# Optimization experiments

Hardware: AMD Instinct MI355X
Metric: run time of the kernel (lower is better)

Reference implementation:

```python
import jax, jax.numpy as jnp
import numpy as np
from jax import lax

EPS_OT = 0.05
N_ITERS = 100
NEG = -1e9

def _l2norm(x):
    n = jnp.sqrt(jnp.sum(x * x, axis=-1, keepdims=True))
    return x / jnp.maximum(n, 1e-12)

def _sinkhorn(C, mu, nu, mask):
    # C: (B, M, Nq); mu: (B, M); nu: (B, Nq); mask: (B, M) bool
    mrow = mask[:, :, None]   # masks rows of K (B,M,Nq)
    mcol = mask[:, None, :]   # masks cols of K^T (B,Nq,M)
    log_mu = jnp.log(mu + 1e-8)
    log_nu = jnp.log(nu + 1e-8)

    def kernel(u, v):
        return (-C + u[:, :, None] + v[:, None, :]) / EPS_OT

    def step(carry, _):
        u, v = carry
        K = jnp.where(mrow, kernel(u, v), NEG)
        u = EPS_OT * (log_mu - jax.scipy.special.logsumexp(K, axis=2)) + u
        Kt = jnp.where(mcol, jnp.transpose(kernel(u, v), (0, 2, 1)), NEG)
        v = EPS_OT * (log_nu - jax.scipy.special.logsumexp(Kt, axis=2)) + v
        return (u, v), None

    u0 = jnp.zeros_like(mu)
    v0 = jnp.zeros_like(nu)
    (u, v), _ = lax.scan(jax.checkpoint(step), (u0, v0), None, length=N_ITERS)
    K = jnp.where(mrow, kernel(u, v), NEG)
    T = jnp.exp(K)
    return jnp.where(mrow, T, 0.0)

def setup_inputs() -> dict:
    key = jax.random.key(0)
    ks = jax.random.split(key, 12)
    Nq, B, M, C = 1024, 8, 1024, 640
    s = 1.0 / np.sqrt(C)
    return {
        "xq": jax.random.normal(ks[0], (Nq, B, C), jnp.float32),
        "xk": jax.random.normal(ks[1], (B, M, C), jnp.float32),
        "xv": jax.random.normal(ks[2], (B, M, C), jnp.float32),
        "mask": jax.random.randint(ks[3], (B, M), 0, 2).astype(bool),
        "Wq": jax.random.normal(ks[4], (C, C), jnp.float32) * s,
        "bq": jnp.zeros((C,), jnp.float32),
        "Wk": jax.random.normal(ks[5], (C, C), jnp.float32) * s,
        "bk": jnp.zeros((C,), jnp.float32),
        "Wv": jax.random.normal(ks[6], (C, C), jnp.float32) * s,
        "bv": jnp.zeros((C,), jnp.float32),
        "Wp": jax.random.normal(ks[7], (C, C), jnp.float32) * s,
        "bp": jnp.zeros((C,), jnp.float32),
    }

def reference(xq, xk, xv, mask, Wq, bq, Wk, bk, Wv, bv, Wp, bp):
    Nq, B, C = xq.shape
    M = xk.shape[1]
    q = _l2norm(xq @ Wq.T + bq)          # (Nq, B, C)
    k = _l2norm(xk @ Wk.T + bk)          # (B, M, C)
    v = xv @ Wv.T + bv                   # (B, M, C)
    # einsum 'bmc,nbc->bnm' then permute(0,2,1) == direct (B, M, Nq)
    sim = jnp.einsum('bmc,nbc->bmn', k, q)
    wdist = 1.0 - sim
    counts = jnp.sum(mask, axis=1, keepdims=True).astype(sim.dtype)  # (B,1)
    xx = mask.astype(sim.dtype) / jnp.maximum(counts, 1.0)
    xx = jnp.where(counts == 0, 1.0 / M, xx)                         # (B, M)
    yy = jnp.full((B, Nq), 1.0 / Nq, sim.dtype)
    T = _sinkhorn(wdist, xx, yy, mask)                               # (B, M, Nq)
    score_map = (M * Nq) * sim * T
    attn_save = jnp.where(mask, jnp.sum(score_map, axis=-1), 0.0)    # (B, M)
    x = jnp.einsum('bmn,bmc->nbc', T, v)                             # (Nq, B, C)
    out = x @ Wp.T + bp
    return out, attn_save
```

## Files before the change

### kernel.cpp

```cpp
#include <hip/hip_runtime.h>
#include <cstdint>
#include <cstddef>

#define B_DIM 8
#define NQ    1024
#define MK    1024
#define CD    640
#define INV_EPS 20.0f
#define EPS_OT  0.05f

typedef unsigned short u16;
typedef __attribute__((ext_vector_type(8))) short bf16x8;
typedef __attribute__((ext_vector_type(4))) float f32x4;

#define GLDS(gp, lp) __builtin_amdgcn_global_load_lds( \
    (const __attribute__((address_space(1))) void*)(gp), \
    (__attribute__((address_space(3))) void*)(lp), 16, 0, 0)

static __device__ __forceinline__ float wave_reduce_sum(float s) {
#pragma unroll
  for (int off = 32; off; off >>= 1) s += __shfl_xor(s, off, 64);
  return s;
}

static __device__ __forceinline__ u16 f2bf(float f) {
  uint32_t u = __float_as_uint(f);
  u += 0x7fff + ((u >> 16) & 1);
  return (u16)(u >> 16);
}

static __device__ __forceinline__ void g_store(float* p, float v) {
  __hip_atomic_store(p, v, __ATOMIC_RELAXED, __HIP_MEMORY_SCOPE_AGENT);
}
static __device__ __forceinline__ float g_load(const float* p) {
  return __hip_atomic_load((float*)p, __ATOMIC_RELAXED, __HIP_MEMORY_SCOPE_AGENT);
}
static __device__ __forceinline__ void g_storeu(unsigned* p, unsigned v) {
  __hip_atomic_store(p, v, __ATOMIC_RELAXED, __HIP_MEMORY_SCOPE_AGENT);
}
static __device__ __forceinline__ unsigned g_loadu(const unsigned* p) {
  return __hip_atomic_load((unsigned*)p, __ATOMIC_RELAXED, __HIP_MEMORY_SCOPE_AGENT);
}

__global__ void k_setup(const void* __restrict__ maskRaw, int* __restrict__ maskI,
                        float* __restrict__ muVal, float* __restrict__ w,
                        unsigned* __restrict__ ctrl)
{
  __shared__ int s_flag;
  __shared__ int s_cnt[B_DIM];
  const int tid = threadIdx.x;
  if (tid == 0) s_flag = 0;
  if (tid < B_DIM) s_cnt[tid] = 0;
  ctrl[tid] = 0u;
  __syncthreads();

  const unsigned char* mb = (const unsigned char*)maskRaw;
  int local = 0;
  for (int i = tid; i < B_DIM * MK; i += 1024)
    if ((i & 3) && mb[i]) local = 1;
  if (local) atomicOr(&s_flag, 1);
  __syncthreads();

  const int isByte = s_flag;
  const int* mi32 = (const int*)maskRaw;
  for (int i = tid; i < B_DIM * MK; i += 1024) {
    int v = isByte ? (int)mb[i] : mi32[i];
    v = v ? 1 : 0;
    maskI[i] = v;
    if (v) atomicAdd(&s_cnt[i >> 10], 1);
  }
  for (int i = tid; i < B_DIM * NQ; i += 1024) w[i] = 1.0f;
  __syncthreads();
  if (tid < B_DIM) {
    float c = (float)s_cnt[tid];
    muVal[tid] = (c > 0.f ? 1.0f / c : 1.0f / (float)MK) + 1e-8f;
  }
}

__global__ __launch_bounds__(256)
void k_cvt5(const float* __restrict__ x0, u16* __restrict__ d0,
            const float* __restrict__ x1, u16* __restrict__ d1,
            const float* __restrict__ x2, u16* __restrict__ d2,
            const float* __restrict__ x3, u16* __restrict__ d3,
            const float* __restrict__ x4, u16* __restrict__ d4)
{
  const int a = blockIdx.y;
  const float* s; u16* d; int n;
  if      (a == 0) { s = x0; d = d0; n = 8192 * CD; }
  else if (a == 1) { s = x1; d = d1; n = 8192 * CD; }
  else if (a == 2) { s = x2; d = d2; n = 8192 * CD; }
  else if (a == 3) { s = x3; d = d3; n = CD * CD; }
  else             { s = x4; d = d4; n = CD * CD; }
  const int i = (blockIdx.x * 256 + threadIdx.x) * 4;
  if (i >= n) return;
  const float4 v = *(const float4*)(s + i);
  *(ushort4*)(d + i) = make_ushort4(f2bf(v.x), f2bf(v.y), f2bf(v.z), f2bf(v.w));
}

__global__ __launch_bounds__(256)
void k_combineA(const float* __restrict__ Wp, const float* __restrict__ Wv,
                u16* __restrict__ Ah)
{
  __shared__ float Ps[32][68];
  __shared__ float Vs[32][68];
  const int tid = threadIdx.x;
  const int c0 = blockIdx.x << 6, k0 = blockIdx.y << 6;
  const int ty = tid >> 4, tx = tid & 15;
  float acc[4][4];
#pragma unroll
  for (int i = 0; i < 4; ++i)
#pragma unroll
    for (int j = 0; j < 4; ++j) acc[i][j] = 0.f;

  for (int j0 = 0; j0 < CD; j0 += 32) {
    {
      const int c = tid >> 2, j4 = (tid & 3) << 3;
      const float* p = Wp + (size_t)(c0 + c) * CD + j0 + j4;
      float4 u0 = *(const float4*)p, u1 = *(const float4*)(p + 4);
      Ps[j4 + 0][c] = u0.x; Ps[j4 + 1][c] = u0.y; Ps[j4 + 2][c] = u0.z; Ps[j4 + 3][c] = u0.w;
      Ps[j4 + 4][c] = u1.x; Ps[j4 + 5][c] = u1.y; Ps[j4 + 6][c] = u1.z; Ps[j4 + 7][c] = u1.w;
    }
    {
      const int j = tid >> 3, k4 = (tid & 7) << 3;
      const float* p = Wv + (size_t)(j0 + j) * CD + k0 + k4;
      float4 u0 = *(const float4*)p, u1 = *(const float4*)(p + 4);
      *(float4*)&Vs[j][k4] = u0; *(float4*)&Vs[j][k4 + 4] = u1;
    }
    __syncthreads();
#pragma unroll
    for (int j = 0; j < 32; ++j) {
      float a[4], b[4];
      *(float4*)a = *(const float4*)&Ps[j][ty << 2];
      *(float4*)b = *(const float4*)&Vs[j][tx << 2];
#pragma unroll
      for (int i = 0; i < 4; ++i)
#pragma unroll
        for (int jj = 0; jj < 4; ++jj)
          acc[i][jj] = fmaf(a[i], b[jj], acc[i][jj]);
    }
    __syncthreads();
  }
#pragma unroll
  for (int i = 0; i < 4; ++i) {
    *(ushort4*)(Ah + (size_t)(c0 + (ty << 2) + i) * CD + k0 + (tx << 2)) =
      make_ushort4(f2bf(acc[i][0]), f2bf(acc[i][1]), f2bf(acc[i][2]), f2bf(acc[i][3]));
  }
}

__global__ __launch_bounds__(256)
void k_bvp(const float* __restrict__ Wp, const float* __restrict__ bv,
           float* __restrict__ bvp)
{
  const int c = (blockIdx.x << 2) + (threadIdx.x >> 6);
  const int lane = threadIdx.x & 63;
  float s = 0.f;
  for (int j = lane; j < CD; j += 64) s = fmaf(Wp[(size_t)c * CD + j], bv[j], s);
  s = wave_reduce_sum(s);
  if (!lane) bvp[c] = s;
}

__global__ __launch_bounds__(256)
void mfma_proj(const u16* __restrict__ xqh, const u16* __restrict__ xkh,
               const u16* __restrict__ xvh,
               const u16* __restrict__ Wqh, const u16* __restrict__ Wkh,
               const u16* __restrict__ Ah,
               const float* __restrict__ bq, const float* __restrict__ bk,
               const float* __restrict__ bvp,
               float* __restrict__ qb, float* __restrict__ kb,
               float* __restrict__ vp)
{
  __shared__ u16 As[128 * 32];
  __shared__ u16 Bs[128 * 32];
  const int mode = blockIdx.z;
  const u16* X     = (mode == 0) ? xqh : ((mode == 1) ? xkh : xvh);
  const u16* W     = (mode == 0) ? Wqh : ((mode == 1) ? Wkh : Ah);
  const float* bias= (mode == 0) ? bq  : ((mode == 1) ? bk  : bvp);
  float* outp      = (mode == 0) ? qb  : ((mode == 1) ? kb  : vp);

  const int tid = threadIdx.x, wave = tid >> 6, lane = tid & 63;
  const int row0 = blockIdx.x << 7, col0 = blockIdx.y << 7;

  const int rS = (wave << 5) + (lane >> 2);
  const int pc = lane & 3;
  const int kc0 = pc ^ ((rS >> 1) & 3);
  const int kc1 = pc ^ (((rS + 16) >> 1) & 3);
  const u16* gA0 = X + (size_t)(row0 + rS) * CD + (kc0 << 3);
  const u16* gA1 = X + (size_t)(row0 + rS + 16) * CD + (kc1 << 3);
  const u16* gB0 = W + (size_t)(col0 + rS) * CD + (kc0 << 3);
  const u16* gB1 = W + (size_t)(col0 + rS + 16) * CD + (kc1 << 3);
  u16* lA = As + (wave << 10);
  u16* lB = Bs + (wave << 10);

  const int wm0 = (wave & 1) << 6, wn0 = (wave >> 1) << 6;
  int aOff[4], bOff[4];
#pragma unroll
  for (int t = 0; t < 4; ++t) {
    const int ra = wm0 + (t << 4) + (lane & 15);
    aOff[t] = ra * 32 + (((lane >> 4) ^ ((ra >> 1) & 3)) << 3);
    const int rb = wn0 + (t << 4) + (lane & 15);
    bOff[t] = rb * 32 + (((lane >> 4) ^ ((rb >> 1) & 3)) << 3);
  }
  f32x4 acc[4][4];
#pragma unroll
  for (int i = 0; i < 4; ++i)
#pragma unroll
    for (int j = 0; j < 4; ++j) acc[i][j] = {0.f, 0.f, 0.f, 0.f};

  for (int k0 = 0; k0 < CD; k0 += 32) {
    __syncthreads();
    GLDS(gA0, lA); GLDS(gA1, lA + 512);
    GLDS(gB0, lB); GLDS(gB1, lB + 512);
    gA0 += 32; gA1 += 32; gB0 += 32; gB1 += 32;
    __syncthreads();
    bf16x8 a[4], b[4];
#pragma unroll
    for (int t = 0; t < 4; ++t) {
      a[t] = *(const bf16x8*)(As + aOff[t]);
      b[t] = *(const bf16x8*)(Bs + bOff[t]);
    }
#pragma unroll
    for (int i = 0; i < 4; ++i)
#pragma unroll
      for (int j = 0; j < 4; ++j)
        acc[i][j] = __builtin_amdgcn_mfma_f32_16x16x32_bf16(a[i], b[j], acc[i][j], 0, 0, 0);
  }

  float bv4[4];
  int ccs[4];
#pragma unroll
  for (int j = 0; j < 4; ++j) {
    ccs[j] = col0 + wn0 + (j << 4) + (lane & 15);
    bv4[j] = bias[ccs[j]];
  }
#pragma unroll
  for (int i = 0; i < 4; ++i) {
    const int rbase = row0 + wm0 + (i << 4) + ((lane >> 4) << 2);
#pragma unroll
    for (int r = 0; r < 4; ++r) {
      const int rr = rbase + r;
      const size_t orow = (mode == 0) ? ((size_t)(rr & 7) * NQ + (rr >> 3)) : (size_t)rr;
      float* op = outp + orow * CD;
#pragma unroll
      for (int j = 0; j < 4; ++j)
        op[ccs[j]] = acc[i][j][r] + bv4[j];
    }
  }
}

__global__ __launch_bounds__(256)
void mfma_sim(const u16* __restrict__ kbh, const u16* __restrict__ qbh,
              float* __restrict__ E)
{
  __shared__ u16 As[128 * 32];
  __shared__ u16 Bs[128 * 32];
  const int tid = threadIdx.x, wave = tid >> 6, lane = tid & 63;
  const int b = blockIdx.z;
  const int row0 = blockIdx.x << 7, col0 = blockIdx.y << 7;
  const u16* A = kbh + (size_t)b * MK * CD;
  const u16* B = qbh + (size_t)b * NQ * CD;

  const int rS = (wave << 5) + (lane >> 2);
  const int pc = lane & 3;
  const int kc0 = pc ^ ((rS >> 1) & 3);
  const int kc1 = pc ^ (((rS + 16) >> 1) & 3);
  const u16* gA0 = A + (size_t)(row0 + rS) * CD + (kc0 << 3);
  const u16* gA1 = A + (size_t)(row0 + rS + 16) * CD + (kc1 << 3);
  const u16* gB0 = B + (size_t)(col0 + rS) * CD + (kc0 << 3);
  const u16* gB1 = B + (size_t)(col0 + rS + 16) * CD + (kc1 << 3);
  u16* lA = As + (wave << 10);
  u16* lB = Bs + (wave << 10);

  const int wm0 = (wave & 1) << 6, wn0 = (wave >> 1) << 6;
  int aOff[4], bOff[4];
#pragma unroll
  for (int t = 0; t < 4; ++t) {
    const int ra = wm0 + (t << 4) + (lane & 15);
    aOff[t] = ra * 32 + (((lane >> 4) ^ ((ra >> 1) & 3)) << 3);
    const int rb = wn0 + (t << 4) + (lane & 15);
    bOff[t] = rb * 32 + (((lane >> 4) ^ ((rb >> 1) & 3)) << 3);
  }
  f32x4 acc[4][4];
#pragma unroll
  for (int i = 0; i < 4; ++i)
#pragma unroll
    for (int j = 0; j < 4; ++j) acc[i][j] = {0.f, 0.f, 0.f, 0.f};

  for (int k0 = 0; k0 < CD; k0 += 32) {
    __syncthreads();
    GLDS(gA0, lA); GLDS(gA1, lA + 512);
    GLDS(gB0, lB); GLDS(gB1, lB + 512);
    gA0 += 32; gA1 += 32; gB0 += 32; gB1 += 32;
    __syncthreads();
    bf16x8 a[4], b[4];
#pragma unroll
    for (int t = 0; t < 4; ++t) {
      a[t] = *(const bf16x8*)(As + aOff[t]);
      b[t] = *(const bf16x8*)(Bs + bOff[t]);
    }
#pragma unroll
    for (int i = 0; i < 4; ++i)
#pragma unroll
      for (int j = 0; j < 4; ++j)
        acc[i][j] = __builtin_amdgcn_mfma_f32_16x16x32_bf16(a[i], b[j], acc[i][j], 0, 0, 0);
  }

#pragma unroll
  for (int i = 0; i < 4; ++i) {
    const int rbase = row0 + wm0 + (i << 4) + ((lane >> 4) << 2);
#pragma unroll
    for (int r = 0; r < 4; ++r) {
      const int rr = rbase + r;
      float* erow = E + (((size_t)(b << 10) + rr) << 10);
#pragma unroll
      for (int j = 0; j < 4; ++j) {
        const int cc = col0 + wn0 + (j << 4) + (lane & 15);
        erow[cc] = __expf((acc[i][j][r] - 1.f) * INV_EPS);
      }
    }
  }
}

__global__ __launch_bounds__(256)
void mfma_x(const u16* __restrict__ Et, const u16* __restrict__ Vpt,
            const float* __restrict__ w, const float* __restrict__ bp,
            float* __restrict__ out)
{
  __shared__ u16 As[128 * 32];
  __shared__ u16 Bs[128 * 32];
  const int tid = threadIdx.x, wave = tid >> 6, lane = tid & 63;
  const int b = blockIdx.z;
  const int row0 = blockIdx.x << 7;
  const int col0 = blockIdx.y << 7;
  const u16* A = Et + ((size_t)b << 20);
  const u16* B = Vpt + (size_t)b * CD * MK;

  const int rS = (wave << 5) + (lane >> 2);
  const int pc = lane & 3;
  const int kc0 = pc ^ ((rS >> 1) & 3);
  const int kc1 = pc ^ (((rS + 16) >> 1) & 3);
  const u16* gA0 = A + ((size_t)(row0 + rS) << 10) + (kc0 << 3);
  const u16* gA1 = A + ((size_t)(row0 + rS + 16) << 10) + (kc1 << 3);
  const u16* gB0 = B + ((size_t)(col0 + rS) << 10) + (kc0 << 3);
  const u16* gB1 = B + ((size_t)(col0 + rS + 16) << 10) + (kc1 << 3);
  u16* lA = As + (wave << 10);
  u16* lB = Bs + (wave << 10);

  const int wm0 = (wave & 1) << 6, wn0 = (wave >> 1) << 6;
  int aOff[4], bOff[4];
#pragma unroll
  for (int t = 0; t < 4; ++t) {
    const int ra = wm0 + (t << 4) + (lane & 15);
    aOff[t] = ra * 32 + (((lane >> 4) ^ ((ra >> 1) & 3)) << 3);
    const int rb = wn0 + (t << 4) + (lane & 15);
    bOff[t] = rb * 32 + (((lane >> 4) ^ ((rb >> 1) & 3)) << 3);
  }
  f32x4 acc[4][4];
#pragma unroll
  for (int i = 0; i < 4; ++i)
#pragma unroll
    for (int j = 0; j < 4; ++j) acc[i][j] = {0.f, 0.f, 0.f, 0.f};

  for (int k0 = 0; k0 < MK; k0 += 32) {
    __syncthreads();
    GLDS(gA0, lA); GLDS(gA1, lA + 512);
    GLDS(gB0, lB); GLDS(gB1, lB + 512);
    gA0 += 32; gA1 += 32; gB0 += 32; gB1 += 32;
    __syncthreads();
    bf16x8 a[4], b[4];
#pragma unroll
    for (int t = 0; t < 4; ++t) {
      a[t] = *(const bf16x8*)(As + aOff[t]);
      b[t] = *(const bf16x8*)(Bs + bOff[t]);
    }
#pragma unroll
    for (int i = 0; i < 4; ++i)
#pragma unroll
      for (int j = 0; j < 4; ++j)
        acc[i][j] = __builtin_amdgcn_mfma_f32_16x16x32_bf16(a[i], b[j], acc[i][j], 0, 0, 0);
  }

  float bv4[4];
  int ccs[4];
#pragma unroll
  for (int j = 0; j < 4; ++j) {
    ccs[j] = col0 + wn0 + (j << 4) + (lane & 15);
    bv4[j] = bp[ccs[j]];
  }
#pragma unroll
  for (int i = 0; i < 4; ++i) {
    const int rbase = row0 + wm0 + (i << 4) + ((lane >> 4) << 2);
#pragma unroll
    for (int r = 0; r < 4; ++r) {
      const int rr = rbase + r;
      const float wn = w[(b << 10) + rr];
      float* op = out + ((size_t)rr * 8 + b) * CD;
#pragma unroll
      for (int j = 0; j < 4; ++j)
        op[ccs[j]] = acc[i][j][r] * wn + bv4[j];
    }
  }
}

__global__ __launch_bounds__(256)
void k_l2bf(const float* __restrict__ X, u16* __restrict__ O)
{
  const int row = (blockIdx.x << 2) + (threadIdx.x >> 6);
  const int lane = threadIdx.x & 63;
  const float2* p2 = (const float2*)(X + (size_t)row * CD);
  float2 v[5];
  float ss = 0.f;
#pragma unroll
  for (int i = 0; i < 5; ++i) {
    v[i] = p2[lane + (i << 6)];
    ss = fmaf(v[i].x, v[i].x, fmaf(v[i].y, v[i].y, ss));
  }
  ss = wave_reduce_sum(ss);
  const float inv = 1.0f / fmaxf(sqrtf(ss), 1e-12f);
  ushort2* o2 = (ushort2*)(O + (size_t)row * CD);
#pragma unroll
  for (int i = 0; i < 5; ++i)
    o2[lane + (i << 6)] = make_ushort2(f2bf(v[i].x * inv), f2bf(v[i].y * inv));
}

__global__ __launch_bounds__(256)
void k_vpt(const float* __restrict__ vp, u16* __restrict__ Vpt)
{
  __shared__ float t[64][65];
  const int b = blockIdx.z, m0 = blockIdx.y << 6, c0 = blockIdx.x << 6;
  const int tid = threadIdx.x;
  const int cc = tid & 63, r4 = tid >> 6;
#pragma unroll
  for (int i = 0; i < 16; ++i) {
    const int m = (i << 2) + r4;
    t[m][cc] = vp[((size_t)((b << 10) + m0 + m)) * CD + c0 + cc];
  }
  __syncthreads();
  const int mm = tid & 63;
#pragma unroll
  for (int i = 0; i < 16; ++i) {
    const int c = (i << 2) + r4;
    Vpt[((size_t)(b * CD + c0 + c) << 10) + m0 + mm] = f2bf(t[mm][c]);
  }
}

__global__ __launch_bounds__(256)
void k_et(const float* __restrict__ E, const float* __restrict__ z,
          u16* __restrict__ Et)
{
  __shared__ float t[64][65];
  const int b = blockIdx.z, m0 = blockIdx.y << 6, n0 = blockIdx.x << 6;
  const int tid = threadIdx.x;
  const int nn = tid & 63, r4 = tid >> 6;
#pragma unroll
  for (int i = 0; i < 16; ++i) {
    const int m = (i << 2) + r4;
    const float zm = z[(b << 10) + m0 + m];
    t[m][nn] = E[(((size_t)((b << 10) + m0 + m)) << 10) + n0 + nn] * zm;
  }
  __syncthreads();
  const int mm = tid & 63;
#pragma unroll
  for (int i = 0; i < 16; ++i) {
    const int n = (i << 2) + r4;
    Et[(((size_t)((b << 10) + n0 + n)) << 10) + m0 + mm] = f2bf(t[mm][n]);
  }
}

__global__ __launch_bounds__(512, 2)
void k_sinkhorn(const float* __restrict__ E, const int* __restrict__ maskI,
                const float* __restrict__ muVal, float* __restrict__ w,
                float* __restrict__ z, float* __restrict__ attn,
                float* __restrict__ part, unsigned* __restrict__ ctrl)
{
  const int b = blockIdx.x & 7;
  const int g = blockIdx.x >> 3;
  const int tid = threadIdx.x;
  const int wave = tid >> 6, lane = tid & 63;
  const int m0 = (g << 6) + (wave << 3);
  const float* Eb = E + ((size_t)b << 20);
  float* wb = w + (b << 10);
  unsigned* flagB = ctrl + 64 + (b << 6);

  __shared__ float wS[1024];
  __shared__ float colRed[8][1024];

  float e[8][16];
#pragma unroll
  for (int r = 0; r < 8; ++r) {
    const float* row = Eb + ((size_t)(m0 + r) << 10) + lane;
#pragma unroll
    for (int j = 0; j < 16; ++j) e[r][j] = row[j << 6];
  }
  float rmask[8];
#pragma unroll
  for (int r = 0; r < 8; ++r)
    rmask[r] = maskI[(b << 10) + m0 + r] ? 1.f : 0.f;
  const float muT = muVal[b];
  const float nuT = 1.0f / (float)NQ + 1e-8f;
  float zr[8];
#pragma unroll
  for (int r = 0; r < 8; ++r) zr[r] = 0.f;

  wS[tid] = 1.0f; wS[tid + 512] = 1.0f;
  __syncthreads();

  for (int it = 0; it < 100; ++it) {
    float* partP = part + (size_t)((((it & 1) << 3) + b) << 14);
    float wv[16];
#pragma unroll
    for (int j = 0; j < 16; ++j) wv[j] = wS[lane + (j << 6)];
#pragma unroll
    for (int r = 0; r < 8; ++r) {
      float s = 0.f;
#pragma unroll
      for (int j = 0; j < 16; ++j) s = fmaf(e[r][j], wv[j], s);
      s = wave_reduce_sum(s);
      zr[r] = rmask[r] * (muT / fmaxf(s, 1e-35f));
    }
#pragma unroll
    for (int j = 0; j < 16; ++j) {
      float pj = 0.f;
#pragma unroll
      for (int r = 0; r < 8; ++r) pj = fmaf(e[r][j], zr[r], pj);
      colRed[wave][lane + (j << 6)] = pj;
    }
    __syncthreads();
    for (int n = tid; n < 1024; n += 512) {
      float s = 0.f;
#pragma unroll
      for (int w8 = 0; w8 < 8; ++w8) s += colRed[w8][n];
      g_store(partP + (g << 10) + n, s);
    }
    __syncthreads();
    const unsigned gen = (unsigned)(it + 1);
    if (tid == 0) g_storeu(flagB + g, gen);
    if (wave == 0 && lane < 16) {
      while (g_loadu(flagB + lane) < gen)
        __builtin_amdgcn_s_sleep(1);
    }
    __syncthreads();
    __builtin_amdgcn_fence(__ATOMIC_ACQUIRE, "workgroup");
    {
      float s0 = 0.f, s1 = 0.f;
#pragma unroll
      for (int gg = 0; gg < 16; ++gg) {
        s0 += g_load(partP + (gg << 10) + tid);
        s1 += g_load(partP + (gg << 10) + tid + 512);
      }
      wS[tid]       = nuT / fmaxf(s0, 1e-35f);
      wS[tid + 512] = nuT / fmaxf(s1, 1e-35f);
    }
    __syncthreads();
  }

  {
    float wv[16];
#pragma unroll
    for (int j = 0; j < 16; ++j) wv[j] = wS[lane + (j << 6)];
#pragma unroll
    for (int r = 0; r < 8; ++r) {
      float s = 0.f;
#pragma unroll
      for (int j = 0; j < 16; ++j) {
        const float ee = e[r][j];
        s += (1.f + EPS_OT * __logf(ee)) * ee * wv[j];
      }
      s = wave_reduce_sum(s);
      if (!lane) {
        const int m = (b << 10) + m0 + r;
        z[m] = zr[r];
        attn[m] = 1048576.0f * zr[r] * s;
      }
    }
    for (int n = tid; n < 1024; n += 512) wb[n] = wS[n];
  }
}

extern "C" void kernel_launch(void* const* d_in, const int* in_sizes, int n_in,
                              void* d_out, int out_size, void* d_ws, size_t ws_size,
                              hipStream_t stream)
{
  const float* xq = (const float*)d_in[0];
  const float* xk = (const float*)d_in[1];
  const float* xv = (const float*)d_in[2];
  const void*  maskRaw = d_in[3];
  const float* Wq = (const float*)d_in[4];
  const float* bq = (const float*)d_in[5];
  const float* Wk = (const float*)d_in[6];
  const float* bk = (const float*)d_in[7];
  const float* Wv = (const float*)d_in[8];
  const float* bv = (const float*)d_in[9];
  const float* Wp = (const float*)d_in[10];
  const float* bp = (const float*)d_in[11];

  float* out  = (float*)d_out;
  float* attn = out + (size_t)NQ * B_DIM * CD;

  char* base = (char*)d_ws;
  const size_t OFF_E   = 0;
  const size_t OFF_QB  = 33554432;
  const size_t OFF_KB  = 54525952;
  const size_t OFF_VP  = 75497472;
  const size_t OFF_VPT = 96468992;
  const size_t OFF_SM  = 106954752;

  float* E   = (float*)(base + OFF_E);
  u16* xqh   = (u16*)(base + OFF_E);
  u16* xkh   = xqh + (size_t)8192 * CD;
  u16* xvh   = xkh + (size_t)8192 * CD;
  float* qb  = (float*)(base + OFF_QB);
  float* part= (float*)(base + OFF_QB);
  u16* Et    = (u16*)(base + OFF_QB + 2097152);
  float* kb  = (float*)(base + OFF_KB);
  float* vp  = (float*)(base + OFF_VP);
  u16* qbh   = (u16*)(base + OFF_VP);
  u16* kbh   = qbh + (size_t)8192 * CD;
  u16* Vpt   = (u16*)(base + OFF_VPT);
  u16* Wqh   = (u16*)(base + OFF_SM);
  u16* Wkh   = Wqh + CD * CD;
  u16* Ah    = Wkh + CD * CD;
  float* bvp = (float*)(Ah + CD * CD);
  float* z   = bvp + CD;
  float* w   = z + B_DIM * MK;
  int* maskI = (int*)(w + B_DIM * NQ);
  float* muVal = (float*)(maskI + B_DIM * MK);
  unsigned* ctrl = (unsigned*)(muVal + B_DIM);

  k_setup<<<1, 1024, 0, stream>>>(maskRaw, maskI, muVal, w, ctrl);
  k_cvt5<<<dim3(5120, 5), 256, 0, stream>>>(xq, xqh, xk, xkh, xv, xvh,
                                            Wq, Wqh, Wk, Wkh);
  k_combineA<<<dim3(10, 10), 256, 0, stream>>>(Wp, Wv, Ah);
  k_bvp<<<160, 256, 0, stream>>>(Wp, bv, bvp);

  mfma_proj<<<dim3(64, 5, 3), 256, 0, stream>>>(xqh, xkh, xvh, Wqh, Wkh, Ah,
                                                bq, bk, bvp, qb, kb, vp);
  k_vpt<<<dim3(10, 16, 8), 256, 0, stream>>>(vp, Vpt);
  k_l2bf<<<4096, 256, 0, stream>>>(qb, qbh);

  mfma_sim<<<dim3(8, 8, 8), 256, 0, stream>>>(kbh, qbh, E);

  {
    void* args[] = {(void*)&E, (void*)&maskI, (void*)&muVal, (void*)&w,
                    (void*)&z, (void*)&attn, (void*)&part, (void*)&ctrl};
    hipLaunchCooperativeKernel((void*)k_sinkhorn, dim3(128), dim3(512),
                               args, 0, stream);
  }

  k_et<<<dim3(16, 16, 8), 256, 0, stream>>>(E, z, Et);
  mfma_x<<<dim3(8, 5, 8), 256, 0, stream>>>(Et, Vpt, w, bp, out);
}
```

Baseline: 738.7 us.

## Fuse V transpose into projection epilogue and shrink mfma_x row tile

The projection kernel's V-mode epilogue now writes bf16 transposed Vpt directly, using packed 4-element stores along M. This removes the fp32 vp intermediate and the separate k_vpt transpose kernel. mfma_x also moves from 128x128 to 64x128 tiles, doubling the grid from 320 to 640 blocks to better fill the GPU's compute units, at the cost of less A/B reuse per block.

```diff
diff --git a/kernel.cpp b/kernel.cpp
--- a/kernel.cpp
+++ b/kernel.cpp
@@ -167,7 +167,7 @@
                const float* __restrict__ bq, const float* __restrict__ bk,
                const float* __restrict__ bvp,
                float* __restrict__ qb, float* __restrict__ kb,
-               float* __restrict__ vp)
+               u16* __restrict__ Vpt)
 {
   __shared__ u16 As[128 * 32];
   __shared__ u16 Bs[128 * 32];
@@ -175,7 +175,6 @@
   const u16* X     = (mode == 0) ? xqh : ((mode == 1) ? xkh : xvh);
   const u16* W     = (mode == 0) ? Wqh : ((mode == 1) ? Wkh : Ah);
   const float* bias= (mode == 0) ? bq  : ((mode == 1) ? bk  : bvp);
-  float* outp      = (mode == 0) ? qb  : ((mode == 1) ? kb  : vp);
 
   const int tid = threadIdx.x, wave = tid >> 6, lane = tid & 63;
   const int row0 = blockIdx.x << 7, col0 = blockIdx.y << 7;
@@ -232,17 +231,32 @@
     ccs[j] = col0 + wn0 + (j << 4) + (lane & 15);
     bv4[j] = bias[ccs[j]];
   }
-#pragma unroll
-  for (int i = 0; i < 4; ++i) {
-    const int rbase = row0 + wm0 + (i << 4) + ((lane >> 4) << 2);
-#pragma unroll
-    for (int r = 0; r < 4; ++r) {
-      const int rr = rbase + r;
-      const size_t orow = (mode == 0) ? ((size_t)(rr & 7) * NQ + (rr >> 3)) : (size_t)rr;
-      float* op = outp + orow * CD;
-#pragma unroll
-      for (int j = 0; j < 4; ++j)
-        op[ccs[j]] = acc[i][j][r] + bv4[j];
+  if (mode == 2) {
+#pragma unroll
+    for (int i = 0; i < 4; ++i) {
+      const int rbase = row0 + wm0 + (i << 4) + ((lane >> 4) << 2);
+      const int bb = rbase >> 10, mloc = rbase & 1023;
+#pragma unroll
+      for (int j = 0; j < 4; ++j) {
+        ushort4 o = make_ushort4(f2bf(acc[i][j][0] + bv4[j]), f2bf(acc[i][j][1] + bv4[j]),
+                                 f2bf(acc[i][j][2] + bv4[j]), f2bf(acc[i][j][3] + bv4[j]));
+        *(ushort4*)(Vpt + (((size_t)(bb * CD + ccs[j])) << 10) + mloc) = o;
+      }
+    }
+  } else {
+    float* outp = (mode == 0) ? qb : kb;
+#pragma unroll
+    for (int i = 0; i < 4; ++i) {
+      const int rbase = row0 + wm0 + (i << 4) + ((lane >> 4) << 2);
+#pragma unroll
+      for (int r = 0; r < 4; ++r) {
+        const int rr = rbase + r;
+        const size_t orow = (mode == 0) ? ((size_t)(rr & 7) * NQ + (rr >> 3)) : (size_t)rr;
+        float* op = outp + orow * CD;
+#pragma unroll
+        for (int j = 0; j < 4; ++j)
+          op[ccs[j]] = acc[i][j][r] + bv4[j];
+      }
     }
   }
 }
@@ -325,78 +339,78 @@
             const float* __restrict__ w, const float* __restrict__ bp,
             float* __restrict__ out)
 {
-  __shared__ u16 As[128 * 32];
+  __shared__ u16 As[64 * 32];
   __shared__ u16 Bs[128 * 32];
   const int tid = threadIdx.x, wave = tid >> 6, lane = tid & 63;
   const int b = blockIdx.z;
-  const int row0 = blockIdx.x << 7;
+  const int row0 = blockIdx.x << 6;
   const int col0 = blockIdx.y << 7;
   const u16* A = Et + ((size_t)b << 20);
   const u16* B = Vpt + (size_t)b * CD * MK;
 
-  const int rS = (wave << 5) + (lane >> 2);
+  const int rA = (wave << 4) + (lane >> 2);
   const int pc = lane & 3;
-  const int kc0 = pc ^ ((rS >> 1) & 3);
-  const int kc1 = pc ^ (((rS + 16) >> 1) & 3);
-  const u16* gA0 = A + ((size_t)(row0 + rS) << 10) + (kc0 << 3);
-  const u16* gA1 = A + ((size_t)(row0 + rS + 16) << 10) + (kc1 << 3);
-  const u16* gB0 = B + ((size_t)(col0 + rS) << 10) + (kc0 << 3);
-  const u16* gB1 = B + ((size_t)(col0 + rS + 16) << 10) + (kc1 << 3);
-  u16* lA = As + (wave << 10);
-  u16* lB = Bs + (wave << 10);
-
-  const int wm0 = (wave & 1) << 6, wn0 = (wave >> 1) << 6;
-  int aOff[4], bOff[4];
+  const int kcA  = pc ^ ((rA >> 1) & 3);
+  const int kcB1 = pc ^ (((rA + 64) >> 1) & 3);
+  const u16* gA0 = A + ((size_t)(row0 + rA) << 10) + (kcA << 3);
+  const u16* gB0 = B + ((size_t)(col0 + rA) << 10) + (kcA << 3);
+  const u16* gB1 = B + ((size_t)(col0 + rA + 64) << 10) + (kcB1 << 3);
+  u16* lA  = As + (wave << 9);
+  u16* lB0 = Bs + (wave << 9);
+  u16* lB1 = Bs + 2048 + (wave << 9);
+
+  int aOff[4], bOff[2];
 #pragma unroll
   for (int t = 0; t < 4; ++t) {
-    const int ra = wm0 + (t << 4) + (lane & 15);
+    const int ra = (t << 4) + (lane & 15);
     aOff[t] = ra * 32 + (((lane >> 4) ^ ((ra >> 1) & 3)) << 3);
-    const int rb = wn0 + (t << 4) + (lane & 15);
+  }
+#pragma unroll
+  for (int t = 0; t < 2; ++t) {
+    const int rb = (wave << 5) + (t << 4) + (lane & 15);
     bOff[t] = rb * 32 + (((lane >> 4) ^ ((rb >> 1) & 3)) << 3);
   }
-  f32x4 acc[4][4];
+  f32x4 acc[4][2];
 #pragma unroll
   for (int i = 0; i < 4; ++i)
 #pragma unroll
-    for (int j = 0; j < 4; ++j) acc[i][j] = {0.f, 0.f, 0.f, 0.f};
+    for (int j = 0; j < 2; ++j) acc[i][j] = {0.f, 0.f, 0.f, 0.f};
 
   for (int k0 = 0; k0 < MK; k0 += 32) {
     __syncthreads();
-    GLDS(gA0, lA); GLDS(gA1, lA + 512);
-    GLDS(gB0, lB); GLDS(gB1, lB + 512);
-    gA0 += 32; gA1 += 32; gB0 += 32; gB1 += 32;
-    __syncthreads();
-    bf16x8 a[4], b[4];
-#pragma unroll
-    for (int t = 0; t < 4; ++t) {
-      a[t] = *(const bf16x8*)(As + aOff[t]);
-      b[t] = *(const bf16x8*)(Bs + bOff[t]);
-    }
+    GLDS(gA0, lA); GLDS(gB0, lB0); GLDS(gB1, lB1);
+    gA0 += 32; gB0 += 32; gB1 += 32;
+    __syncthreads();
+    bf16x8 a[4], b[2];
+#pragma unroll
+    for (int t = 0; t < 4; ++t) a[t] = *(const bf16x8*)(As + aOff[t]);
+#pragma unroll
+    for (int t = 0; t < 2; ++t) b[t] = *(const bf16x8*)(Bs + bOff[t]);
 #pragma unroll
     for (int i = 0; i < 4; ++i)
 #pragma unroll
-      for (int j = 0; j < 4; ++j)
+      for (int j = 0; j < 2; ++j)
         acc[i][j] = __builtin_amdgcn_mfma_f32_16x16x32_bf16(a[i], b[j], acc[i][j], 0, 0, 0);
   }
 
-  float bv4[4];
-  int ccs[4];
-#pragma unroll
-  for (int j = 0; j < 4; ++j) {
-    ccs[j] = col0 + wn0 + (j << 4) + (lane & 15);
-    bv4[j] = bp[ccs[j]];
+  float bv2[2];
+  int ccs[2];
+#pragma unroll
+  for (int j = 0; j < 2; ++j) {
+    ccs[j] = col0 + (wave << 5) + (j << 4) + (lane & 15);
+    bv2[j] = bp[ccs[j]];
   }
 #pragma unroll
   for (int i = 0; i < 4; ++i) {
-    const int rbase = row0 + wm0 + (i << 4) + ((lane >> 4) << 2);
+    const int rbase = row0 + (i << 4) + ((lane >> 4) << 2);
 #pragma unroll
     for (int r = 0; r < 4; ++r) {
       const int rr = rbase + r;
       const float wn = w[(b << 10) + rr];
       float* op = out + ((size_t)rr * 8 + b) * CD;
 #pragma unroll
-      for (int j = 0; j < 4; ++j)
-        op[ccs[j]] = acc[i][j][r] * wn + bv4[j];
+      for (int j = 0; j < 2; ++j)
+        op[ccs[j]] = acc[i][j][r] * wn + bv2[j];
     }
   }
 }
@@ -420,27 +434,6 @@
 #pragma unroll
   for (int i = 0; i < 5; ++i)
     o2[lane + (i << 6)] = make_ushort2(f2bf(v[i].x * inv), f2bf(v[i].y * inv));
-}
-
-__global__ __launch_bounds__(256)
-void k_vpt(const float* __restrict__ vp, u16* __restrict__ Vpt)
-{
-  __shared__ float t[64][65];
-  const int b = blockIdx.z, m0 = blockIdx.y << 6, c0 = blockIdx.x << 6;
-  const int tid = threadIdx.x;
-  const int cc = tid & 63, r4 = tid >> 6;
-#pragma unroll
-  for (int i = 0; i < 16; ++i) {
-    const int m = (i << 2) + r4;
-    t[m][cc] = vp[((size_t)((b << 10) + m0 + m)) * CD + c0 + cc];
-  }
-  __syncthreads();
-  const int mm = tid & 63;
-#pragma unroll
-  for (int i = 0; i < 16; ++i) {
-    const int c = (i << 2) + r4;
-    Vpt[((size_t)(b * CD + c0 + c) << 10) + m0 + mm] = f2bf(t[mm][c]);
-  }
 }
 
 __global__ __launch_bounds__(256)
@@ -612,7 +605,6 @@
   float* part= (float*)(base + OFF_QB);
   u16* Et    = (u16*)(base + OFF_QB + 2097152);
   float* kb  = (float*)(base + OFF_KB);
-  float* vp  = (float*)(base + OFF_VP);
   u16* qbh   = (u16*)(base + OFF_VP);
   u16* kbh   = qbh + (size_t)8192 * CD;
   u16* Vpt   = (u16*)(base + OFF_VPT);
@@ -633,8 +625,7 @@
   k_bvp<<<160, 256, 0, stream>>>(Wp, bv, bvp);
 
   mfma_proj<<<dim3(64, 5, 3), 256, 0, stream>>>(xqh, xkh, xvh, Wqh, Wkh, Ah,
-                                                bq, bk, bvp, qb, kb, vp);
-  k_vpt<<<dim3(10, 16, 8), 256, 0, stream>>>(vp, Vpt);
+                                                bq, bk, bvp, qb, kb, Vpt);
   k_l2bf<<<4096, 256, 0, stream>>>(qb, qbh);
 
   mfma_sim<<<dim3(8, 8, 8), 256, 0, stream>>>(kbh, qbh, E);
@@ -647,5 +638,5 @@
   }
 
   k_et<<<dim3(16, 16, 8), 256, 0, stream>>>(E, z, Et);
-  mfma_x<<<dim3(8, 5, 8), 256, 0, stream>>>(Et, Vpt, w, bp, out);
-}
+  mfma_x<<<dim3(16, 5, 8), 256, 0, stream>>>(Et, Vpt, w, bp, out);
+}
```

New measurement: 727.3 us. Within noise of the previous version (-1.5%).
